# Performance work log

Measured on AMD Instinct MI355X. Metric: run time of the kernel, lower is better.

The kernel has to match this reference:

```python
import jax, jax.numpy as jnp
import numpy as np

V_F_LEN = 512
I_F_LEN = 256
F_LEN = V_F_LEN + I_F_LEN  # 768, GRU input_size == hidden_size == f_len
NUM_LAYERS = 2
B, S = 64, 256


def _uniform(key, shape, scale):
    return jax.random.uniform(key, shape, jnp.float32, -scale, scale)


def setup_inputs() -> dict:
    key = jax.random.key(0)
    ks = jax.random.split(key, 16)
    fv = jax.random.normal(ks[0], (B, S, V_F_LEN), jnp.float32)
    fi = jax.random.normal(ks[1], (B, S, I_F_LEN), jnp.float32)
    ts = jax.random.uniform(ks[2], (B, S), jnp.float32)
    H = F_LEN
    sc = 1.0 / np.sqrt(H)
    # GRU params, PyTorch layout: [num_layers, 3H, H] with gate order (r, z, n)
    W_ih = _uniform(ks[3], (NUM_LAYERS, 3 * H, H), sc)
    W_hh = _uniform(ks[4], (NUM_LAYERS, 3 * H, H), sc)
    b_ih = _uniform(ks[5], (NUM_LAYERS, 3 * H), sc)
    b_hh = _uniform(ks[6], (NUM_LAYERS, 3 * H), sc)
    sc1 = 1.0 / np.sqrt(H)
    sc2 = 1.0 / np.sqrt(128)
    W1 = _uniform(ks[7], (128, H), sc1)
    b1 = _uniform(ks[8], (128,), sc1)
    W2 = _uniform(ks[9], (6, 128), sc2)
    b2 = _uniform(ks[10], (6,), sc2)
    return {"fv": fv, "fi": fi, "ts": ts, "W_ih": W_ih, "W_hh": W_hh,
            "b_ih": b_ih, "b_hh": b_hh, "W1": W1, "b1": b1, "W2": W2, "b2": b2}


def _gru_layer(x, h0, Wih, Whh, bih, bhh):
    # x: [B, S, H], h0: [B, H]
    def step(h, x_t):
        gi = x_t @ Wih.T + bih          # [B, 3H]
        gh = h @ Whh.T + bhh
        ir, iz, in_ = jnp.split(gi, 3, axis=-1)
        hr, hz, hn = jnp.split(gh, 3, axis=-1)
        r = jax.nn.sigmoid(ir + hr)
        z = jax.nn.sigmoid(iz + hz)
        n = jnp.tanh(in_ + r * hn)
        h_new = (1.0 - z) * n + z * h
        return h_new, h_new
    h_last, ys = jax.lax.scan(step, h0, jnp.swapaxes(x, 0, 1))  # ys: [S, B, H]
    return jnp.swapaxes(ys, 0, 1), h_last


def reference(fv, fi, ts, W_ih, W_hh, b_ih, b_hh, W1, b1, W2, b2):
    # FusionModule with fuse_method='cat': concatenate along feature dim
    fused = jnp.concatenate([fv, fi], axis=-1)  # [B, S, F_LEN]
    bsz = fused.shape[0]
    h0 = jnp.zeros((NUM_LAYERS, bsz, F_LEN), fused.dtype)
    # Note: the torch module feeds one timestep at a time, but the math is
    # identical to running the full sequence through the multilayer GRU.
    x = fused
    h_finals = []
    for l in range(NUM_LAYERS):
        x, h_l = _gru_layer(x, h0[l], W_ih[l], W_hh[l], b_ih[l], b_hh[l])
        h_finals.append(h_l)
    h_n = jnp.stack(h_finals, axis=0)  # [L, B, H]
    hdn = x @ W1.T + b1
    hdn = jnp.where(hdn >= 0, hdn, 0.1 * hdn)  # LeakyReLU(0.1)
    pose = hdn @ W2.T + b2                      # [B, S, 6]
    return (pose, h_n)
```

## Files before the change

### kernel.cpp

```cpp
#include <hip/hip_runtime.h>
#include <stdint.h>


typedef __attribute__((ext_vector_type(8))) short bf16x8;
typedef __attribute__((ext_vector_type(4))) short bf16x4;
typedef __attribute__((ext_vector_type(4))) float f32x4;

#define H_   768
#define TH3  2304
#define BATCH 64
#define SEQ  256
#define SLAB (BATCH * H_)
#define WROW 772
#define FL_STRIDE 256

__device__ __forceinline__ uint16_t f2b(float f) {
  union { float f; uint32_t u; } v; v.f = f;
  uint32_t u = v.u;
  return (uint16_t)((u + 0x7FFFu + ((u >> 16) & 1u)) >> 16);
}

__device__ __forceinline__ f32x4 mfma16(bf16x8 a, bf16x8 b, f32x4 c) {
  return __builtin_amdgcn_mfma_f32_16x16x32_bf16(a, b, c, 0, 0, 0);
}

__device__ __forceinline__ bf16x8 ldB(const uint16_t* p) {
  bf16x4 lo = *reinterpret_cast<const bf16x4*>(p);
  bf16x4 hi = *reinterpret_cast<const bf16x4*>(p + 4);
  bf16x8 r;
  r[0] = lo[0]; r[1] = lo[1]; r[2] = lo[2]; r[3] = lo[3];
  r[4] = hi[0]; r[5] = hi[1]; r[6] = hi[2]; r[7] = hi[3];
  return r;
}

__global__ __launch_bounds__(256) void prep_kernel(
    const float* __restrict__ fv, const float* __restrict__ fi,
    const float* __restrict__ W1,
    uint16_t* __restrict__ Xbf, uint16_t* __restrict__ Y0, uint16_t* __restrict__ Y1,
    int* __restrict__ flags, uint16_t* __restrict__ W1b)
{
  const int NX = SEQ * SLAB;
  const int NY = SLAB;
  const int NC = 257 * FL_STRIDE;
  const int NW = 128 * H_;
  const int total = NX + 2 * NY + NC + NW;
  for (int idx = blockIdx.x * blockDim.x + threadIdx.x; idx < total;
       idx += gridDim.x * blockDim.x) {
    if (idx < NX) {
      int s = idx / SLAB;
      int rem = idx - s * SLAB;
      int b = rem / H_;
      int h = rem - b * H_;
      float val = (h < 512) ? fv[((size_t)b * SEQ + s) * 512 + h]
                            : fi[((size_t)b * SEQ + s) * 256 + (h - 512)];
      Xbf[idx] = f2b(val);
    } else if (idx < NX + 2 * NY) {
      int k = idx - NX;
      if (k < NY) Y0[k] = 0; else Y1[k - NY] = 0;
    } else if (idx < NX + 2 * NY + NC) {
      flags[idx - NX - 2 * NY] = 0;
    } else {
      int k = idx - NX - 2 * NY - NC;
      W1b[k] = f2b(W1[k]);
    }
  }
}

__global__ __launch_bounds__(256) void gru_persist(
    const float* __restrict__ Wih, const float* __restrict__ Whh,
    const float* __restrict__ bih, const float* __restrict__ bhh,
    const uint16_t* __restrict__ Xbf, uint16_t* __restrict__ Y0, uint16_t* __restrict__ Y1,
    int* __restrict__ flags, float* __restrict__ out_hn)
{
  __shared__ __attribute__((aligned(16))) uint16_t Wx[48 * WROW];
  __shared__ __attribute__((aligned(16))) uint16_t Wh[48 * WROW];
  __shared__ float ghbuf[32 * 48];
  __shared__ float hmast[32 * 16];
  __shared__ float bI[48];
  __shared__ float bH[48];

  const int bid   = blockIdx.x;
  const int slice = bid % 48;
  const int layer = (bid / 48) & 1;
  const int bhalf = bid / 96;
  const int tid  = threadIdx.x;
  const int lane = tid & 63;
  const int wid  = tid >> 6;
  const int mblk = wid & 1;
  const int isGh = wid >> 1;
  const int n16  = lane & 15;
  const int kg   = lane >> 4;

  const float* wx_g = Wih + (size_t)layer * TH3 * H_;
  const float* wh_g = Whh + (size_t)layer * TH3 * H_;
  for (int idx = tid; idx < 48 * H_; idx += 256) {
    int lr = idx / H_;
    int c  = idx - lr * H_;
    int gate = lr >> 4, j = lr & 15;
    size_t grow = (size_t)(gate * H_ + slice * 16 + j);
    Wx[lr * WROW + c] = f2b(wx_g[grow * H_ + c]);
    Wh[lr * WROW + c] = f2b(wh_g[grow * H_ + c]);
  }
  if (tid < 48) {
    int gate = tid >> 4, j = tid & 15;
    bI[tid] = bih[layer * TH3 + gate * H_ + slice * 16 + j];
    bH[tid] = bhh[layer * TH3 + gate * H_ + slice * 16 + j];
  }
  for (int idx = tid; idx < 32 * 16; idx += 256) hmast[idx] = 0.0f;
  __syncthreads();

  const int batch0 = bhalf * 32;
  uint16_t* Yown = layer ? Y1 : Y0;

  for (int r = 0; r <= 256; ++r) {
    const bool active = (layer == 0) ? (r < 256) : (r >= 1);
    f32x4 acc0 = {0,0,0,0}, acc1 = {0,0,0,0}, acc2 = {0,0,0,0};
    uint16_t* dst = nullptr;

    if (active) {
      const uint16_t* xs = (layer == 0) ? (Xbf + (size_t)r * SLAB) : (Y0 + (size_t)r * SLAB);
      const uint16_t* hs = (layer == 0) ? (Y0 + (size_t)r * SLAB) : (Y1 + (size_t)(r - 1) * SLAB);
      dst = Yown + (size_t)((layer == 0) ? (r + 1) : r) * SLAB;

      const int* fb = nullptr;
      if (r >= 1) {
        if (isGh)            fb = flags + (size_t)(r - 1) * FL_STRIDE + bhalf * 96 + layer * 48;
        else if (layer == 1) fb = flags + (size_t)(r - 1) * FL_STRIDE + bhalf * 96;
      }
      if (fb) {
        const int* fp = fb + (lane < 48 ? lane : 0);
        int spins = 0;
        for (;;) {
          int v = __hip_atomic_load(fp, __ATOMIC_RELAXED, __HIP_MEMORY_SCOPE_AGENT);
          if (lane >= 48) v = 1;
          if (__all(v != 0)) break;
          if (++spins > (1 << 15)) break;
          __builtin_amdgcn_s_sleep(1);
        }
      }

      const uint16_t* A  = (isGh ? hs : xs) + (size_t)(batch0 + mblk * 16) * H_;
      const uint16_t* ap = A + (size_t)n16 * H_ + kg * 8;
      const uint16_t* Wl = isGh ? Wh : Wx;
      const uint16_t* bp = Wl + (size_t)n16 * WROW + kg * 8;

      #pragma unroll
      for (int ks = 0; ks < 24; ++ks) {
        bf16x8 av  = *reinterpret_cast<const bf16x8*>(ap + ks * 32);
        bf16x8 bv0 = ldB(bp + ks * 32);
        bf16x8 bv1 = ldB(bp + 16 * WROW + ks * 32);
        bf16x8 bv2 = ldB(bp + 32 * WROW + ks * 32);
        acc0 = mfma16(av, bv0, acc0);
        acc1 = mfma16(av, bv1, acc1);
        acc2 = mfma16(av, bv2, acc2);
      }
      if (isGh) {
        #pragma unroll
        for (int q = 0; q < 4; ++q) {
          int bi = mblk * 16 + 4 * kg + q;
          ghbuf[bi * 48 +      n16] = acc0[q];
          ghbuf[bi * 48 + 16 + n16] = acc1[q];
          ghbuf[bi * 48 + 32 + n16] = acc2[q];
        }
      }
    }
    __syncthreads();

    if (active && !isGh) {
      const bool lastStep = (layer == 0) ? (r == 255) : (r == 256);
      #pragma unroll
      for (int q = 0; q < 4; ++q) {
        int bi = mblk * 16 + 4 * kg + q;
        float ghr = ghbuf[bi * 48 +      n16] + bH[n16];
        float ghz = ghbuf[bi * 48 + 16 + n16] + bH[16 + n16];
        float ghn = ghbuf[bi * 48 + 32 + n16] + bH[32 + n16];
        float gxr = acc0[q] + bI[n16];
        float gxz = acc1[q] + bI[16 + n16];
        float gxn = acc2[q] + bI[32 + n16];
        float rg = 1.0f / (1.0f + __expf(-(gxr + ghr)));
        float zg = 1.0f / (1.0f + __expf(-(gxz + ghz)));
        float ng = tanhf(gxn + rg * ghn);
        float hv = hmast[bi * 16 + n16];
        float hn2 = (1.0f - zg) * ng + zg * hv;
        hmast[bi * 16 + n16] = hn2;
        uint32_t lo = (uint32_t)f2b(hn2);
        uint32_t partner = (uint32_t)__shfl_xor((int)lo, 1, 64);
        if ((n16 & 1) == 0) {
          uint32_t pack = lo | (partner << 16);
          uint32_t* p = (uint32_t*)(dst + (size_t)(batch0 + bi) * H_ + slice * 16 + n16);
          __hip_atomic_store(p, pack, __ATOMIC_RELAXED, __HIP_MEMORY_SCOPE_AGENT);
        }
        if (lastStep)
          out_hn[(size_t)layer * SLAB + (size_t)(batch0 + bi) * H_ + slice * 16 + n16] = hn2;
      }
      __builtin_amdgcn_s_waitcnt(0);
    }

    __syncthreads();

    if (r < 256 && tid == 0)
      __hip_atomic_store(&flags[(size_t)r * FL_STRIDE + bid], 1, __ATOMIC_RELAXED,
                         __HIP_MEMORY_SCOPE_AGENT);
  }
}

__global__ __launch_bounds__(256) void regressor_kernel(
    const uint16_t* __restrict__ Y1, const uint16_t* __restrict__ W1b,
    const float* __restrict__ b1, const float* __restrict__ W2,
    const float* __restrict__ b2, float* __restrict__ pose)
{
  __shared__ float hdn[64 * 132];
  const int t = blockIdx.x;
  const int tid = threadIdx.x;
  const int lane = tid & 63;
  const int wid = tid >> 6;
  const int n16 = lane & 15;
  const int kg = lane >> 4;

  const uint16_t* A  = Y1 + (size_t)(t + 1) * SLAB + (size_t)(wid * 16) * H_;
  const uint16_t* ap = A + (size_t)n16 * H_ + kg * 8;
  const uint16_t* bp = W1b + (size_t)n16 * H_ + kg * 8;

  f32x4 acc[8];
  #pragma unroll
  for (int i = 0; i < 8; ++i) acc[i] = (f32x4){0,0,0,0};

  #pragma unroll
  for (int ks = 0; ks < 24; ++ks) {
    bf16x8 av = *reinterpret_cast<const bf16x8*>(ap + ks * 32);
    #pragma unroll
    for (int nt = 0; nt < 8; ++nt) {
      bf16x8 bv = *reinterpret_cast<const bf16x8*>(bp + (size_t)nt * 16 * H_ + ks * 32);
      acc[nt] = mfma16(av, bv, acc[nt]);
    }
  }
  #pragma unroll
  for (int nt = 0; nt < 8; ++nt) {
    #pragma unroll
    for (int q = 0; q < 4; ++q) {
      int brow = wid * 16 + 4 * kg + q;
      int col  = nt * 16 + n16;
      float v = acc[nt][q] + b1[col];
      v = (v >= 0.0f) ? v : 0.1f * v;
      hdn[brow * 132 + col] = v;
    }
  }
  __syncthreads();
  for (int idx = tid; idx < 384; idx += 256) {
    int b = idx / 6, o = idx % 6;
    const float* w2r = W2 + o * 128;
    const float* hr  = &hdn[b * 132];
    float s = b2[o];
    #pragma unroll 4
    for (int c = 0; c < 128; ++c) s += hr[c] * w2r[c];
    pose[(size_t)b * (SEQ * 6) + (size_t)t * 6 + o] = s;
  }
}

extern "C" void kernel_launch(void* const* d_in, const int* in_sizes, int n_in,
                              void* d_out, int out_size, void* d_ws, size_t ws_size,
                              hipStream_t stream) {
  const float* fv  = (const float*)d_in[0];
  const float* fi  = (const float*)d_in[1];
  const float* Wih = (const float*)d_in[3];
  const float* Whh = (const float*)d_in[4];
  const float* bih = (const float*)d_in[5];
  const float* bhh = (const float*)d_in[6];
  const float* W1  = (const float*)d_in[7];
  const float* b1  = (const float*)d_in[8];
  const float* W2  = (const float*)d_in[9];
  const float* b2  = (const float*)d_in[10];
  float* out = (float*)d_out;

  char* ws = (char*)d_ws;
  size_t off = 0;
  int* flags = (int*)(ws + off);
  off += (size_t)257 * FL_STRIDE * sizeof(int);
  off = (off + 255) & ~(size_t)255;
  uint16_t* Xbf = (uint16_t*)(ws + off); off += (size_t)SEQ * SLAB * 2;
  uint16_t* Y0  = (uint16_t*)(ws + off); off += (size_t)257 * SLAB * 2;
  uint16_t* Y1  = (uint16_t*)(ws + off); off += (size_t)257 * SLAB * 2;
  uint16_t* W1b = (uint16_t*)(ws + off); off += (size_t)128 * H_ * 2;

  prep_kernel<<<2048, 256, 0, stream>>>(fv, fi, W1, Xbf, Y0, Y1, flags, W1b);
  gru_persist<<<192, 256, 0, stream>>>(Wih, Whh, bih, bhh, Xbf, Y0, Y1, flags, out + 98304);
  regressor_kernel<<<SEQ, 256, 0, stream>>>(Y1, W1b, b1, W2, b2, out);
}
```

Before: 2.244 ms.

## Use per-wave flags and double-buffered gh to drop block barrier in GRU

Readiness flags are now published per wave and per 16-batch sub-block instead of once per block after a second __syncthreads, so consumers poll only the rows they need. The gh scratch buffer is double-buffered, which removes the trailing barrier of each timestep. The first step skips the h@Whh GEMM and zero-fills gh instead of reading zeroed Y buffers, so the prep kernel no longer clears Y0/Y1. This shortens the critical path of the sequential recurrence at the cost of more flag traffic and subtler ordering between waves.

Measured after the change: 2.391 ms. 6.5% more time.

```diff
diff --git a/kernel.cpp b/kernel.cpp
--- a/kernel.cpp
+++ b/kernel.cpp
@@ -12,7 +12,7 @@
 #define SEQ  256
 #define SLAB (BATCH * H_)
 #define WROW 772
-#define FL_STRIDE 256
+#define FL_ROUND 512
 
 __device__ __forceinline__ uint16_t f2b(float f) {
   union { float f; uint32_t u; } v; v.f = f;
@@ -33,17 +33,32 @@
   return r;
 }
 
+__device__ __forceinline__ int fidx(int i, int m, int grp, int slice) {
+  return ((i * 2 + m) * 4 + grp) * 64 + slice;
+}
+
+__device__ __forceinline__ void pollFlags(const int* base, int lane) {
+  const int* fp = base + (lane < 48 ? lane : 0);
+  int spins = 0;
+  for (;;) {
+    int v = __hip_atomic_load(fp, __ATOMIC_RELAXED, __HIP_MEMORY_SCOPE_AGENT);
+    if (lane >= 48) v = 1;
+    if (__all(v != 0)) break;
+    if (++spins > (1 << 15)) break;
+    __builtin_amdgcn_s_sleep(1);
+  }
+  __builtin_amdgcn_sched_barrier(0);
+}
+
 __global__ __launch_bounds__(256) void prep_kernel(
     const float* __restrict__ fv, const float* __restrict__ fi,
     const float* __restrict__ W1,
-    uint16_t* __restrict__ Xbf, uint16_t* __restrict__ Y0, uint16_t* __restrict__ Y1,
-    int* __restrict__ flags, uint16_t* __restrict__ W1b)
+    uint16_t* __restrict__ Xbf, int* __restrict__ flags, uint16_t* __restrict__ W1b)
 {
   const int NX = SEQ * SLAB;
-  const int NY = SLAB;
-  const int NC = 257 * FL_STRIDE;
+  const int NC = 257 * FL_ROUND;
   const int NW = 128 * H_;
-  const int total = NX + 2 * NY + NC + NW;
+  const int total = NX + NC + NW;
   for (int idx = blockIdx.x * blockDim.x + threadIdx.x; idx < total;
        idx += gridDim.x * blockDim.x) {
     if (idx < NX) {
@@ -54,13 +69,10 @@
       float val = (h < 512) ? fv[((size_t)b * SEQ + s) * 512 + h]
                             : fi[((size_t)b * SEQ + s) * 256 + (h - 512)];
       Xbf[idx] = f2b(val);
-    } else if (idx < NX + 2 * NY) {
-      int k = idx - NX;
-      if (k < NY) Y0[k] = 0; else Y1[k - NY] = 0;
-    } else if (idx < NX + 2 * NY + NC) {
-      flags[idx - NX - 2 * NY] = 0;
+    } else if (idx < NX + NC) {
+      flags[idx - NX] = 0;
     } else {
-      int k = idx - NX - 2 * NY - NC;
+      int k = idx - NX - NC;
       W1b[k] = f2b(W1[k]);
     }
   }
@@ -74,7 +86,7 @@
 {
   __shared__ __attribute__((aligned(16))) uint16_t Wx[48 * WROW];
   __shared__ __attribute__((aligned(16))) uint16_t Wh[48 * WROW];
-  __shared__ float ghbuf[32 * 48];
+  __shared__ float ghbuf[2][32 * 48];
   __shared__ float hmast[32 * 16];
   __shared__ float bI[48];
   __shared__ float bH[48];
@@ -83,6 +95,7 @@
   const int slice = bid % 48;
   const int layer = (bid / 48) & 1;
   const int bhalf = bid / 96;
+  const int grp   = bhalf * 2 + layer;
   const int tid  = threadIdx.x;
   const int lane = tid & 63;
   const int wid  = tid >> 6;
@@ -111,72 +124,84 @@
 
   const int batch0 = bhalf * 32;
   uint16_t* Yown = layer ? Y1 : Y0;
-
-  for (int r = 0; r <= 256; ++r) {
-    const bool active = (layer == 0) ? (r < 256) : (r >= 1);
-    f32x4 acc0 = {0,0,0,0}, acc1 = {0,0,0,0}, acc2 = {0,0,0,0};
-    uint16_t* dst = nullptr;
+  const uint16_t* Wl_h = Wh + (size_t)n16 * WROW + kg * 8;
+  const uint16_t* Wl_x = Wx + (size_t)n16 * WROW + kg * 8;
+
+  f32x4 xac0 = {0,0,0,0}, xac1 = {0,0,0,0}, xac2 = {0,0,0,0};
+
+  for (int i = 0; i <= 256; ++i) {
+    const bool active = (layer == 0) ? (i < 256) : (i >= 1);
+    const bool firstA = (layer == 0) ? (i == 0) : (i == 1);
+    float* gb = ghbuf[i & 1];
 
     if (active) {
-      const uint16_t* xs = (layer == 0) ? (Xbf + (size_t)r * SLAB) : (Y0 + (size_t)r * SLAB);
-      const uint16_t* hs = (layer == 0) ? (Y0 + (size_t)r * SLAB) : (Y1 + (size_t)(r - 1) * SLAB);
-      dst = Yown + (size_t)((layer == 0) ? (r + 1) : r) * SLAB;
-
-      const int* fb = nullptr;
-      if (r >= 1) {
-        if (isGh)            fb = flags + (size_t)(r - 1) * FL_STRIDE + bhalf * 96 + layer * 48;
-        else if (layer == 1) fb = flags + (size_t)(r - 1) * FL_STRIDE + bhalf * 96;
+      if (isGh) {
+        if (firstA) {
+          #pragma unroll
+          for (int q = 0; q < 4; ++q) {
+            int bi = mblk * 16 + 4 * kg + q;
+            gb[bi * 48 +      n16] = 0.0f;
+            gb[bi * 48 + 16 + n16] = 0.0f;
+            gb[bi * 48 + 32 + n16] = 0.0f;
+          }
+        } else {
+          pollFlags(flags + fidx(i - 1, mblk, grp, 0), lane);
+          const uint16_t* hs = (layer == 0) ? (Y0 + (size_t)i * SLAB)
+                                            : (Y1 + (size_t)(i - 1) * SLAB);
+          const uint16_t* ap = hs + (size_t)(batch0 + mblk * 16 + n16) * H_ + kg * 8;
+          f32x4 a0 = {0,0,0,0}, a1 = {0,0,0,0}, a2 = {0,0,0,0};
+          #pragma unroll
+          for (int ks = 0; ks < 24; ++ks) {
+            bf16x8 av  = *reinterpret_cast<const bf16x8*>(ap + ks * 32);
+            bf16x8 bv0 = ldB(Wl_h + ks * 32);
+            bf16x8 bv1 = ldB(Wl_h + 16 * WROW + ks * 32);
+            bf16x8 bv2 = ldB(Wl_h + 32 * WROW + ks * 32);
+            a0 = mfma16(av, bv0, a0);
+            a1 = mfma16(av, bv1, a1);
+            a2 = mfma16(av, bv2, a2);
+          }
+          #pragma unroll
+          for (int q = 0; q < 4; ++q) {
+            int bi = mblk * 16 + 4 * kg + q;
+            gb[bi * 48 +      n16] = a0[q];
+            gb[bi * 48 + 16 + n16] = a1[q];
+            gb[bi * 48 + 32 + n16] = a2[q];
+          }
+        }
+      } else {
+        if (layer == 1) pollFlags(flags + fidx(i - 1, mblk, bhalf * 2, 0), lane);
+        const uint16_t* xs = (layer == 0) ? (Xbf + (size_t)i * SLAB)
+                                          : (Y0 + (size_t)i * SLAB);
+        const uint16_t* ap = xs + (size_t)(batch0 + mblk * 16 + n16) * H_ + kg * 8;
+        f32x4 a0 = {0,0,0,0}, a1 = {0,0,0,0}, a2 = {0,0,0,0};
+        #pragma unroll
+        for (int ks = 0; ks < 24; ++ks) {
+          bf16x8 av  = *reinterpret_cast<const bf16x8*>(ap + ks * 32);
+          bf16x8 bv0 = ldB(Wl_x + ks * 32);
+          bf16x8 bv1 = ldB(Wl_x + 16 * WROW + ks * 32);
+          bf16x8 bv2 = ldB(Wl_x + 32 * WROW + ks * 32);
+          a0 = mfma16(av, bv0, a0);
+          a1 = mfma16(av, bv1, a1);
+          a2 = mfma16(av, bv2, a2);
+        }
+        xac0 = a0; xac1 = a1; xac2 = a2;
       }
-      if (fb) {
-        const int* fp = fb + (lane < 48 ? lane : 0);
-        int spins = 0;
-        for (;;) {
-          int v = __hip_atomic_load(fp, __ATOMIC_RELAXED, __HIP_MEMORY_SCOPE_AGENT);
-          if (lane >= 48) v = 1;
-          if (__all(v != 0)) break;
-          if (++spins > (1 << 15)) break;
-          __builtin_amdgcn_s_sleep(1);
-        }
-      }
-
-      const uint16_t* A  = (isGh ? hs : xs) + (size_t)(batch0 + mblk * 16) * H_;
-      const uint16_t* ap = A + (size_t)n16 * H_ + kg * 8;
-      const uint16_t* Wl = isGh ? Wh : Wx;
-      const uint16_t* bp = Wl + (size_t)n16 * WROW + kg * 8;
-
-      #pragma unroll
-      for (int ks = 0; ks < 24; ++ks) {
-        bf16x8 av  = *reinterpret_cast<const bf16x8*>(ap + ks * 32);
-        bf16x8 bv0 = ldB(bp + ks * 32);
-        bf16x8 bv1 = ldB(bp + 16 * WROW + ks * 32);
-        bf16x8 bv2 = ldB(bp + 32 * WROW + ks * 32);
-        acc0 = mfma16(av, bv0, acc0);
-        acc1 = mfma16(av, bv1, acc1);
-        acc2 = mfma16(av, bv2, acc2);
-      }
-      if (isGh) {
-        #pragma unroll
-        for (int q = 0; q < 4; ++q) {
-          int bi = mblk * 16 + 4 * kg + q;
-          ghbuf[bi * 48 +      n16] = acc0[q];
-          ghbuf[bi * 48 + 16 + n16] = acc1[q];
-          ghbuf[bi * 48 + 32 + n16] = acc2[q];
-        }
-      }
-    }
+    }
+
     __syncthreads();
 
     if (active && !isGh) {
-      const bool lastStep = (layer == 0) ? (r == 255) : (r == 256);
+      uint16_t* dst = Yown + (size_t)((layer == 0) ? (i + 1) : i) * SLAB;
+      const bool lastStep = (layer == 0) ? (i == 255) : (i == 256);
       #pragma unroll
       for (int q = 0; q < 4; ++q) {
         int bi = mblk * 16 + 4 * kg + q;
-        float ghr = ghbuf[bi * 48 +      n16] + bH[n16];
-        float ghz = ghbuf[bi * 48 + 16 + n16] + bH[16 + n16];
-        float ghn = ghbuf[bi * 48 + 32 + n16] + bH[32 + n16];
-        float gxr = acc0[q] + bI[n16];
-        float gxz = acc1[q] + bI[16 + n16];
-        float gxn = acc2[q] + bI[32 + n16];
+        float ghr = gb[bi * 48 +      n16] + bH[n16];
+        float ghz = gb[bi * 48 + 16 + n16] + bH[16 + n16];
+        float ghn = gb[bi * 48 + 32 + n16] + bH[32 + n16];
+        float gxr = xac0[q] + bI[n16];
+        float gxz = xac1[q] + bI[16 + n16];
+        float gxn = xac2[q] + bI[32 + n16];
         float rg = 1.0f / (1.0f + __expf(-(gxr + ghr)));
         float zg = 1.0f / (1.0f + __expf(-(gxz + ghz)));
         float ng = tanhf(gxn + rg * ghn);
@@ -194,13 +219,11 @@
           out_hn[(size_t)layer * SLAB + (size_t)(batch0 + bi) * H_ + slice * 16 + n16] = hn2;
       }
       __builtin_amdgcn_s_waitcnt(0);
-    }
-
-    __syncthreads();
-
-    if (r < 256 && tid == 0)
-      __hip_atomic_store(&flags[(size_t)r * FL_STRIDE + bid], 1, __ATOMIC_RELAXED,
-                         __HIP_MEMORY_SCOPE_AGENT);
+      __builtin_amdgcn_sched_barrier(0);
+      if (lane == 0)
+        __hip_atomic_store(&flags[fidx(i, mblk, grp, slice)], 1, __ATOMIC_RELAXED,
+                           __HIP_MEMORY_SCOPE_AGENT);
+    }
   }
 }
 
@@ -275,14 +298,14 @@
   char* ws = (char*)d_ws;
   size_t off = 0;
   int* flags = (int*)(ws + off);
-  off += (size_t)257 * FL_STRIDE * sizeof(int);
+  off += (size_t)257 * FL_ROUND * sizeof(int);
   off = (off + 255) & ~(size_t)255;
   uint16_t* Xbf = (uint16_t*)(ws + off); off += (size_t)SEQ * SLAB * 2;
   uint16_t* Y0  = (uint16_t*)(ws + off); off += (size_t)257 * SLAB * 2;
   uint16_t* Y1  = (uint16_t*)(ws + off); off += (size_t)257 * SLAB * 2;
   uint16_t* W1b = (uint16_t*)(ws + off); off += (size_t)128 * H_ * 2;
 
-  prep_kernel<<<2048, 256, 0, stream>>>(fv, fi, W1, Xbf, Y0, Y1, flags, W1b);
+  prep_kernel<<<2048, 256, 0, stream>>>(fv, fi, W1, Xbf, flags, W1b);
   gru_persist<<<192, 256, 0, stream>>>(Wih, Whh, bih, bhh, Xbf, Y0, Y1, flags, out + 98304);
   regressor_kernel<<<SEQ, 256, 0, stream>>>(Y1, W1b, b1, W2, b2, out);
 }
```
